# Performance work log

Hardware: AMD Instinct MI355X
Metric: run time of the kernel (lower is better)

## Reference

```python
import jax, jax.numpy as jnp
import numpy as np

IN_DIM = 128
LAYER_DIMS = [128, 128]
NUM_SAMPLES = [25, 10]
L0 = 3072
NEG_WEIGHT = 1.0


def setup_inputs() -> dict:
    key = jax.random.key(0)
    ks = jax.random.split(key, 12)
    feat = jax.random.normal(ks[0], (L0, IN_DIM), dtype=jnp.float32)
    nodes = jax.random.randint(ks[1], (L0,), 0, L0)
    nb0 = jnp.arange(L0)
    nb1 = jax.random.randint(ks[2], (L0 * 10,), 0, L0)
    nb2 = jax.random.randint(ks[3], (L0 * 10 * 25,), 0, L0)
    src_idx = jax.random.randint(ks[4], (1024,), 0, L0)
    pos_idx = jax.random.randint(ks[5], (1024,), 0, L0)
    neg_idx = jax.random.randint(ks[6], (512,), 0, L0)
    g = 0.05
    # mean aggregator weights: layer0 in=IN_DIM, layer1 in=2*128 (concat)
    w_self_0 = jax.random.normal(ks[7], (IN_DIM, 128), jnp.float32) * g
    w_neigh_0 = jax.random.normal(ks[8], (IN_DIM, 128), jnp.float32) * g
    w_self_1 = jax.random.normal(ks[9], (256, 128), jnp.float32) * g
    w_neigh_1 = jax.random.normal(ks[10], (256, 128), jnp.float32) * g
    return dict(nodes=nodes, feat=feat, src_idx=src_idx, pos_idx=pos_idx,
                neg_idx=neg_idx, nb0=nb0, nb1=nb1, nb2=nb2,
                w_self_0=w_self_0, w_neigh_0=w_neigh_0,
                w_self_1=w_self_1, w_neigh_1=w_neigh_1)


def _aggregate(hidden, params):
    # GraphSAGE layer stack: at layer l, combine each hop with the mean of its
    # sampled neighbors, concat self/neigh transforms, relu except last layer.
    num_layers = len(NUM_SAMPLES)
    for layer in range(num_layers):
        w_self, w_neigh = params[layer]
        is_last = layer == num_layers - 1
        next_hidden = []
        for hop in range(num_layers - layer):
            s = NUM_SAMPLES[num_layers - hop - 1]
            self_v = hidden[hop]  # [n, d]
            neigh = hidden[hop + 1].reshape(self_v.shape[0], s, self_v.shape[1])
            neigh_mean = jnp.mean(neigh, axis=1)
            h = jnp.concatenate([self_v @ w_self, neigh_mean @ w_neigh], axis=1)
            if not is_last:
                h = jax.nn.relu(h)
            next_hidden.append(h)
        hidden = next_hidden
    return hidden[0]


def _l2_normalize(x, eps=1e-12):
    return x * jax.lax.rsqrt(jnp.maximum(jnp.sum(x * x, axis=1, keepdims=True), eps))


def reference(nodes, feat, src_idx, pos_idx, neg_idx, nb0, nb1, nb2,
              w_self_0, w_neigh_0, w_self_1, w_neigh_1):
    hidden = [feat[nb0], feat[nb1], feat[nb2]]
    params = [(w_self_0, w_neigh_0), (w_self_1, w_neigh_1)]
    output = _aggregate(hidden, params)          # [L0, 256]
    output = _l2_normalize(output)
    src_emb = output[src_idx]                    # [B, 256]
    pos_emb = output[pos_idx]
    neg_emb = output[neg_idx]                    # [Nneg, 256]

    aff = jnp.sum(src_emb * pos_emb, axis=1)     # [B]
    neg_aff = src_emb @ neg_emb.T                # [B, Nneg]

    # MRR via double argsort (tf double top_k equivalent; ties -> positive last)
    aff_all = jnp.concatenate([neg_aff, aff[:, None]], axis=1)
    order = jnp.argsort(-aff_all, axis=1, stable=True)
    ranks = jnp.argsort(order, axis=1, stable=True)
    mrr = jnp.mean(1.0 / (ranks[:, -1].astype(jnp.float32) + 1.0))

    # sigmoid cross-entropy: labels 1 -> softplus(-x); labels 0 -> softplus(x)
    true_xent = jax.nn.softplus(-aff)
    neg_xent = jax.nn.softplus(neg_aff)
    loss = jnp.sum(true_xent) + NEG_WEIGHT * jnp.sum(neg_xent)
    loss = loss / jnp.asarray(src_emb.shape[0], jnp.float32)
    return src_emb, loss, mrr
```

## Files before the change

### kernel.cpp

```cpp
#include <hip/hip_runtime.h>
#include <math.h>

#define L0      3072
#define DIM     128
#define BATCH   1024
#define NNEG    512


__device__ __forceinline__ float bf2f(unsigned short u) {
  return __uint_as_float(((unsigned)u) << 16);
}
__device__ __forceinline__ void store_out(float v, float* p) { *p = v; }
__device__ __forceinline__ void store_out(float v, unsigned short* p) {
  unsigned x = __float_as_uint(v);
  *p = (unsigned short)((x + 0x7fff + ((x >> 16) & 1)) >> 16);
}

template<int K, int AW, int HOFF, bool NORM, typename OutT>
__global__ __launch_bounds__(256) void k_mm(
    const float* __restrict__ Ain,
    const float* __restrict__ W0, const float* __restrict__ W1,
    OutT* __restrict__ Out, const int ldo, const int outHalfOff,
    float* __restrict__ zbuf, const int zcount) {
  __shared__ float AT[6 * AW];
  __shared__ float rs[4][3];
  const int t = threadIdx.x;
  if (zbuf != nullptr && blockIdx.x == 0)
    for (int z = t; z < zcount; z += 256) zbuf[z] = 0.f;
  const int base = blockIdx.x * 6;
  {
    const float4* __restrict__ src = (const float4*)(Ain + base * AW);
    float4* __restrict__ dst = (float4*)AT;
    for (int idx = t; idx < 6 * AW / 4; idx += 256) dst[idx] = src[idx];
  }
  __syncthreads();

  const int half = t >> 7;
  const int rg = ((t >> 6) & 1) * 3;
  const int c = t & 63;
  const float* __restrict__ W = (half ? W1 : W0) + c;
  const float* __restrict__ A0 = AT + rg * AW + half * HOFF;

  float acc[3][2];
#pragma unroll
  for (int r = 0; r < 3; ++r) { acc[r][0] = 0.f; acc[r][1] = 0.f; }

#pragma unroll 4
  for (int d = 0; d < K; d += 4) {
    float4 a[3];
#pragma unroll
    for (int r = 0; r < 3; ++r) a[r] = *(const float4*)&A0[r * AW + d];
    float w0[4], w1[4];
#pragma unroll
    for (int i2 = 0; i2 < 4; ++i2) {
      w0[i2] = W[(d + i2) * 128];
      w1[i2] = W[(d + i2) * 128 + 64];
    }
#pragma unroll
    for (int i2 = 0; i2 < 4; ++i2)
#pragma unroll
      for (int r = 0; r < 3; ++r) {
        const float av = ((const float*)&a[r])[i2];
        acc[r][0] = fmaf(av, w0[i2], acc[r][0]);
        acc[r][1] = fmaf(av, w1[i2], acc[r][1]);
      }
  }

  float scale[3] = {1.f, 1.f, 1.f};
  if (NORM) {
    float p[3];
#pragma unroll
    for (int r = 0; r < 3; ++r) p[r] = acc[r][0] * acc[r][0] + acc[r][1] * acc[r][1];
#pragma unroll
    for (int off = 32; off > 0; off >>= 1)
#pragma unroll
      for (int r = 0; r < 3; ++r) p[r] += __shfl_xor(p[r], off, 64);
    const int wv = t >> 6;
    if ((t & 63) == 0) { rs[wv][0] = p[0]; rs[wv][1] = p[1]; rs[wv][2] = p[2]; }
    __syncthreads();
#pragma unroll
    for (int r = 0; r < 3; ++r) {
      const float s = (rg == 0) ? (rs[0][r] + rs[2][r]) : (rs[1][r] + rs[3][r]);
      scale[r] = rsqrtf(fmaxf(s, 1e-12f));
    }
  }
  OutT* __restrict__ O = Out + half * outHalfOff + c;
#pragma unroll
  for (int r = 0; r < 3; ++r) {
    store_out(acc[r][0] * scale[r], &O[(base + rg + r) * ldo]);
    store_out(acc[r][1] * scale[r], &O[(base + rg + r) * ldo + 64]);
  }
}

__global__ __launch_bounds__(640) void k_aggregate(
    const unsigned short* __restrict__ X0, const unsigned short* __restrict__ Y0,
    const int* __restrict__ nb0, const int* __restrict__ nb1,
    const int* __restrict__ nb2, float* __restrict__ H) {
  __shared__ int idxs[260];
  __shared__ float gB[10][128], gC[10][128], gD[10][128];
  const int i = blockIdx.x;
  const int t = threadIdx.x;
  if (t < 250) idxs[t] = nb2[i * 250 + t];
  else if (t < 260) idxs[t] = nb1[i * 10 + t - 250];
  __syncthreads();

  const int j = t >> 6;
  const int lam = t & 63;
  const int c8 = lam & 15;
  const int sub = lam >> 4;
  const int* __restrict__ pj = idxs + j * 25;

  float d8[8];
#pragma unroll
  for (int e = 0; e < 8; ++e) d8[e] = 0.f;
#pragma unroll
  for (int m = 0; m < 7; ++m) {
    const int k = sub + 4 * m;
    if (k < 25) {
      const int r = pj[k];
      const float4 raw = *(const float4*)(Y0 + r * 128 + c8 * 8);
      const unsigned short* u = (const unsigned short*)&raw;
#pragma unroll
      for (int e = 0; e < 8; ++e) d8[e] += bf2f(u[e]);
    }
  }
#pragma unroll
  for (int e = 0; e < 8; ++e) d8[e] += __shfl_xor(d8[e], 16, 64);
#pragma unroll
  for (int e = 0; e < 8; ++e) d8[e] += __shfl_xor(d8[e], 32, 64);

  const int r1 = idxs[250 + j];
  if (sub == 0) {
#pragma unroll
    for (int e = 0; e < 8; ++e) gD[j][c8 * 8 + e] = fmaxf(d8[e] * 0.04f, 0.f);
    const float4 raw = *(const float4*)(Y0 + r1 * 128 + c8 * 8);
    const unsigned short* u = (const unsigned short*)&raw;
#pragma unroll
    for (int e = 0; e < 8; ++e) gB[j][c8 * 8 + e] = bf2f(u[e]);
  } else if (sub == 1) {
    const float4 raw = *(const float4*)(X0 + r1 * 128 + c8 * 8);
    const unsigned short* u = (const unsigned short*)&raw;
#pragma unroll
    for (int e = 0; e < 8; ++e) gC[j][c8 * 8 + e] = fmaxf(bf2f(u[e]), 0.f);
  }
  __syncthreads();

  if (t < 512) {
    const int q = t >> 7, c = t & 127;
    float v;
    if (q == 0) {
      v = fmaxf(bf2f(X0[nb0[i] * 128 + c]), 0.f);
    } else {
      const float* g = (q == 1) ? &gB[0][0] : (q == 2) ? &gC[0][0] : &gD[0][0];
      float s = 0.f;
#pragma unroll
      for (int jj = 0; jj < 10; ++jj) s += g[jj * 128 + c];
      v = s * 0.1f;
      if (q == 1) v = fmaxf(v, 0.f);
    }
    H[i * 512 + t] = v;
  }
}

__device__ __forceinline__ float softplusf(float x) {
  return fmaxf(x, 0.f) + log1pf(expf(-fabsf(x)));
}

__global__ __launch_bounds__(64) void k_aff(
    const float* __restrict__ O, const int* __restrict__ src_idx,
    const int* __restrict__ pos_idx, float* __restrict__ out_src,
    float* __restrict__ aff, float* __restrict__ spPos) {
  __shared__ float4 sv[64], pv[64];
  const int b = blockIdx.x;
  const int q = threadIdx.x;
  const int s = src_idx[b];
  const int p = pos_idx[b];
  float4 vs = ((const float4*)O)[s * 64 + q];
  ((float4*)out_src)[b * 64 + q] = vs;
  sv[q] = vs;
  pv[q] = ((const float4*)O)[p * 64 + q];
  __syncthreads();
  if (q == 0) {
    const float* __restrict__ ss = (const float*)sv;
    const float* __restrict__ pp = (const float*)pv;
    float a = 0.f;
#pragma unroll 16
    for (int d = 0; d < 256; ++d) a = fmaf(ss[d], pp[d], a);
    aff[b] = a;
    atomicAdd(spPos, softplusf(-a));
  }
}

__global__ __launch_bounds__(256) void k_neg(
    const float* __restrict__ O, const int* __restrict__ src_idx,
    const int* __restrict__ neg_idx, const float* __restrict__ aff,
    int* __restrict__ rank, float* __restrict__ spNeg) {
  __shared__ float SL[32][129];
  __shared__ float NL[64][129];
  __shared__ float affL[32];
  __shared__ int cntL[32];
  const int t = threadIdx.x;
  const int rowBase = (blockIdx.x >> 3) * 32;
  const int colBase = (blockIdx.x & 7) * 64;
  if (t < 32) { affL[t] = aff[rowBase + t]; cntL[t] = 0; }
  const int ct = t & 31;
  const int rt = t >> 5;
  float acc[4][2];
#pragma unroll
  for (int k = 0; k < 4; ++k) { acc[k][0] = 0.f; acc[k][1] = 0.f; }
  for (int ch = 0; ch < 2; ++ch) {
    __syncthreads();
    for (int idx = t; idx < 32 * 128; idx += 256) {
      int r = idx >> 7, dd = idx & 127;
      SL[r][dd] = O[src_idx[rowBase + r] * 256 + ch * 128 + dd];
    }
    for (int idx = t; idx < 64 * 128; idx += 256) {
      int cpos = idx >> 7, dd = idx & 127;
      NL[cpos][dd] = O[neg_idx[colBase + cpos] * 256 + ch * 128 + dd];
    }
    __syncthreads();
    for (int dd = 0; dd < 128; ++dd) {
      float n0 = NL[ct][dd], n1 = NL[ct + 32][dd];
#pragma unroll
      for (int k = 0; k < 4; ++k) {
        float sv = SL[rt + 8 * k][dd];
        acc[k][0] = fmaf(sv, n0, acc[k][0]);
        acc[k][1] = fmaf(sv, n1, acc[k][1]);
      }
    }
  }
  float sp = 0.f;
#pragma unroll
  for (int k = 0; k < 4; ++k) {
    float a = affL[rt + 8 * k];
    int cnt = 0;
#pragma unroll
    for (int cc = 0; cc < 2; ++cc) {
      float v = acc[k][cc];
      sp += softplusf(v);
      cnt += (v >= a) ? 1 : 0;
    }
    if (cnt) atomicAdd(&cntL[rt + 8 * k], cnt);
  }
#pragma unroll
  for (int off = 32; off > 0; off >>= 1) sp += __shfl_down(sp, off, 64);
  if ((t & 63) == 0) atomicAdd(spNeg, sp);
  __syncthreads();
  if (t < 32) atomicAdd(&rank[rowBase + t], cntL[t]);
}

__global__ __launch_bounds__(256) void k_finalize(
    const int* __restrict__ rank, const float* __restrict__ spPos,
    const float* __restrict__ spNeg, float* __restrict__ out) {
  const int t = threadIdx.x;
  float s = 0.f;
  for (int i = t; i < BATCH; i += 256) s += 1.f / (float)(rank[i] + 1);
#pragma unroll
  for (int off = 32; off > 0; off >>= 1) s += __shfl_down(s, off, 64);
  __shared__ float wsum[4];
  if ((t & 63) == 0) wsum[t >> 6] = s;
  __syncthreads();
  if (t == 0) {
    float mrr = (wsum[0] + wsum[1] + wsum[2] + wsum[3]) * (1.f / 1024.f);
    float loss = (spPos[0] + spNeg[0]) * (1.f / 1024.f);
    out[BATCH * 256]     = loss;
    out[BATCH * 256 + 1] = mrr;
  }
}

extern "C" void kernel_launch(void* const* d_in, const int* in_sizes, int n_in,
                              void* d_out, int out_size, void* d_ws, size_t ws_size,
                              hipStream_t stream) {
  const float* feat   = (const float*)d_in[1];
  const int* src_idx  = (const int*)d_in[2];
  const int* pos_idx  = (const int*)d_in[3];
  const int* neg_idx  = (const int*)d_in[4];
  const int* nb0      = (const int*)d_in[5];
  const int* nb1      = (const int*)d_in[6];
  const int* nb2      = (const int*)d_in[7];
  const float* ws0    = (const float*)d_in[8];
  const float* wn0    = (const float*)d_in[9];
  const float* ws1    = (const float*)d_in[10];
  const float* wn1    = (const float*)d_in[11];

  float* wsf = (float*)d_ws;
  unsigned short* X0 = (unsigned short*)d_ws;
  unsigned short* Y0 = X0 + 393216;
  float* H     = wsf + 393216;
  float* R     = wsf + 1966080;
  float* aff   = wsf + 2752512;
  float* spPos = wsf + 2753536;
  float* spNeg = wsf + 2753537;
  int*   rank  = (int*)(wsf + 2753538);
  float* out   = (float*)d_out;

  k_mm<128, 128, 0, false, unsigned short><<<L0 / 6, 256, 0, stream>>>(
      feat, ws0, wn0, X0, 128, 393216, spPos, 1026);
  k_aggregate<<<L0, 640, 0, stream>>>(X0, Y0, nb0, nb1, nb2, H);
  k_mm<256, 512, 256, true, float><<<L0 / 6, 256, 0, stream>>>(
      H, ws1, wn1, R, 256, 128, nullptr, 0);
  k_aff<<<BATCH, 64, 0, stream>>>(R, src_idx, pos_idx, out, aff, spPos);
  k_neg<<<(BATCH / 32) * (NNEG / 64), 256, 0, stream>>>(R, src_idx, neg_idx, aff, rank, spNeg);
  k_finalize<<<1, 256, 0, stream>>>(rank, spPos, spNeg, out);
}
```

Before: 182.7 us.

## Fuse affinity kernel into k_neg, widen k_mm to 512 threads, shuffle indices

Removes the separate k_aff launch. Each k_neg block now recomputes the positive affinity for its 32 rows, and the first column block writes the src embeddings and accumulates the positive softplus. k_mm doubles its threads to 512, so each thread computes one output column instead of two, which raises parallelism and cuts registers per thread. k_aggregate replaces the shared-memory index staging and its barrier with per-wave register loads broadcast via __shfl. The cost is redundant affinity dot products across the 8 column blocks, done serially by 32 threads with strided global reads.

```diff
diff --git a/kernel.cpp b/kernel.cpp
--- a/kernel.cpp
+++ b/kernel.cpp
@@ -2,7 +2,6 @@
 #include <math.h>
 
 #define L0      3072
-#define DIM     128
 #define BATCH   1024
 #define NNEG    512
 
@@ -17,98 +16,88 @@
 }
 
 template<int K, int AW, int HOFF, bool NORM, typename OutT>
-__global__ __launch_bounds__(256) void k_mm(
+__global__ __launch_bounds__(512) void k_mm(
     const float* __restrict__ Ain,
     const float* __restrict__ W0, const float* __restrict__ W1,
     OutT* __restrict__ Out, const int ldo, const int outHalfOff,
     float* __restrict__ zbuf, const int zcount) {
   __shared__ float AT[6 * AW];
-  __shared__ float rs[4][3];
+  __shared__ float rs[8][3];
   const int t = threadIdx.x;
   if (zbuf != nullptr && blockIdx.x == 0)
-    for (int z = t; z < zcount; z += 256) zbuf[z] = 0.f;
+    for (int z = t; z < zcount; z += 512) zbuf[z] = 0.f;
   const int base = blockIdx.x * 6;
   {
     const float4* __restrict__ src = (const float4*)(Ain + base * AW);
     float4* __restrict__ dst = (float4*)AT;
-    for (int idx = t; idx < 6 * AW / 4; idx += 256) dst[idx] = src[idx];
-  }
-  __syncthreads();
-
-  const int half = t >> 7;
-  const int rg = ((t >> 6) & 1) * 3;
-  const int c = t & 63;
-  const float* __restrict__ W = (half ? W1 : W0) + c;
+    for (int idx = t; idx < 6 * AW / 4; idx += 512) dst[idx] = src[idx];
+  }
+  __syncthreads();
+
+  const int wave = t >> 6;
+  const int half = wave >> 2;
+  const int colg = (wave >> 1) & 1;
+  const int rowg = wave & 1;
+  const int rg = rowg * 3;
+  const int col = colg * 64 + (t & 63);
+  const float* __restrict__ W = (half ? W1 : W0) + col;
   const float* __restrict__ A0 = AT + rg * AW + half * HOFF;
 
-  float acc[3][2];
-#pragma unroll
-  for (int r = 0; r < 3; ++r) { acc[r][0] = 0.f; acc[r][1] = 0.f; }
-
+  float acc[3] = {0.f, 0.f, 0.f};
 #pragma unroll 4
   for (int d = 0; d < K; d += 4) {
     float4 a[3];
 #pragma unroll
     for (int r = 0; r < 3; ++r) a[r] = *(const float4*)&A0[r * AW + d];
-    float w0[4], w1[4];
-#pragma unroll
-    for (int i2 = 0; i2 < 4; ++i2) {
-      w0[i2] = W[(d + i2) * 128];
-      w1[i2] = W[(d + i2) * 128 + 64];
-    }
+    float w[4];
+#pragma unroll
+    for (int i2 = 0; i2 < 4; ++i2) w[i2] = W[(d + i2) * 128];
 #pragma unroll
     for (int i2 = 0; i2 < 4; ++i2)
 #pragma unroll
-      for (int r = 0; r < 3; ++r) {
-        const float av = ((const float*)&a[r])[i2];
-        acc[r][0] = fmaf(av, w0[i2], acc[r][0]);
-        acc[r][1] = fmaf(av, w1[i2], acc[r][1]);
-      }
+      for (int r = 0; r < 3; ++r)
+        acc[r] = fmaf(((const float*)&a[r])[i2], w[i2], acc[r]);
   }
 
   float scale[3] = {1.f, 1.f, 1.f};
   if (NORM) {
     float p[3];
 #pragma unroll
-    for (int r = 0; r < 3; ++r) p[r] = acc[r][0] * acc[r][0] + acc[r][1] * acc[r][1];
+    for (int r = 0; r < 3; ++r) p[r] = acc[r] * acc[r];
 #pragma unroll
     for (int off = 32; off > 0; off >>= 1)
 #pragma unroll
       for (int r = 0; r < 3; ++r) p[r] += __shfl_xor(p[r], off, 64);
-    const int wv = t >> 6;
-    if ((t & 63) == 0) { rs[wv][0] = p[0]; rs[wv][1] = p[1]; rs[wv][2] = p[2]; }
+    if ((t & 63) == 0) { rs[wave][0] = p[0]; rs[wave][1] = p[1]; rs[wave][2] = p[2]; }
     __syncthreads();
 #pragma unroll
     for (int r = 0; r < 3; ++r) {
-      const float s = (rg == 0) ? (rs[0][r] + rs[2][r]) : (rs[1][r] + rs[3][r]);
+      const float s = rs[rowg][r] + rs[rowg + 2][r] + rs[rowg + 4][r] + rs[rowg + 6][r];
       scale[r] = rsqrtf(fmaxf(s, 1e-12f));
     }
   }
-  OutT* __restrict__ O = Out + half * outHalfOff + c;
-#pragma unroll
-  for (int r = 0; r < 3; ++r) {
-    store_out(acc[r][0] * scale[r], &O[(base + rg + r) * ldo]);
-    store_out(acc[r][1] * scale[r], &O[(base + rg + r) * ldo + 64]);
-  }
+  OutT* __restrict__ O = Out + half * outHalfOff;
+#pragma unroll
+  for (int r = 0; r < 3; ++r)
+    store_out(acc[r] * scale[r], &O[(base + rg + r) * ldo + col]);
 }
 
 __global__ __launch_bounds__(640) void k_aggregate(
     const unsigned short* __restrict__ X0, const unsigned short* __restrict__ Y0,
     const int* __restrict__ nb0, const int* __restrict__ nb1,
     const int* __restrict__ nb2, float* __restrict__ H) {
-  __shared__ int idxs[260];
   __shared__ float gB[10][128], gC[10][128], gD[10][128];
   const int i = blockIdx.x;
   const int t = threadIdx.x;
-  if (t < 250) idxs[t] = nb2[i * 250 + t];
-  else if (t < 260) idxs[t] = nb1[i * 10 + t - 250];
-  __syncthreads();
-
+  const int n0 = nb0[i];
   const int j = t >> 6;
   const int lam = t & 63;
+  const int r = i * 10 + j;
+  int myidx = 0;
+  if (lam < 25) myidx = nb2[r * 25 + lam];
+  else if (lam == 25) myidx = nb1[r];
   const int c8 = lam & 15;
   const int sub = lam >> 4;
-  const int* __restrict__ pj = idxs + j * 25;
 
   float d8[8];
 #pragma unroll
@@ -116,9 +105,9 @@
 #pragma unroll
   for (int m = 0; m < 7; ++m) {
     const int k = sub + 4 * m;
+    const int ridx = __shfl(myidx, k, 64);
     if (k < 25) {
-      const int r = pj[k];
-      const float4 raw = *(const float4*)(Y0 + r * 128 + c8 * 8);
+      const float4 raw = *(const float4*)(Y0 + ridx * 128 + c8 * 8);
       const unsigned short* u = (const unsigned short*)&raw;
 #pragma unroll
       for (int e = 0; e < 8; ++e) d8[e] += bf2f(u[e]);
@@ -129,7 +118,7 @@
 #pragma unroll
   for (int e = 0; e < 8; ++e) d8[e] += __shfl_xor(d8[e], 32, 64);
 
-  const int r1 = idxs[250 + j];
+  const int r1 = __shfl(myidx, 25, 64);
   if (sub == 0) {
 #pragma unroll
     for (int e = 0; e < 8; ++e) gD[j][c8 * 8 + e] = fmaxf(d8[e] * 0.04f, 0.f);
@@ -149,7 +138,7 @@
     const int q = t >> 7, c = t & 127;
     float v;
     if (q == 0) {
-      v = fmaxf(bf2f(X0[nb0[i] * 128 + c]), 0.f);
+      v = fmaxf(bf2f(X0[n0 * 128 + c]), 0.f);
     } else {
       const float* g = (q == 1) ? &gB[0][0] : (q == 2) ? &gC[0][0] : &gD[0][0];
       float s = 0.f;
@@ -166,35 +155,11 @@
   return fmaxf(x, 0.f) + log1pf(expf(-fabsf(x)));
 }
 
-__global__ __launch_bounds__(64) void k_aff(
-    const float* __restrict__ O, const int* __restrict__ src_idx,
-    const int* __restrict__ pos_idx, float* __restrict__ out_src,
-    float* __restrict__ aff, float* __restrict__ spPos) {
-  __shared__ float4 sv[64], pv[64];
-  const int b = blockIdx.x;
-  const int q = threadIdx.x;
-  const int s = src_idx[b];
-  const int p = pos_idx[b];
-  float4 vs = ((const float4*)O)[s * 64 + q];
-  ((float4*)out_src)[b * 64 + q] = vs;
-  sv[q] = vs;
-  pv[q] = ((const float4*)O)[p * 64 + q];
-  __syncthreads();
-  if (q == 0) {
-    const float* __restrict__ ss = (const float*)sv;
-    const float* __restrict__ pp = (const float*)pv;
-    float a = 0.f;
-#pragma unroll 16
-    for (int d = 0; d < 256; ++d) a = fmaf(ss[d], pp[d], a);
-    aff[b] = a;
-    atomicAdd(spPos, softplusf(-a));
-  }
-}
-
 __global__ __launch_bounds__(256) void k_neg(
     const float* __restrict__ O, const int* __restrict__ src_idx,
-    const int* __restrict__ neg_idx, const float* __restrict__ aff,
-    int* __restrict__ rank, float* __restrict__ spNeg) {
+    const int* __restrict__ pos_idx, const int* __restrict__ neg_idx,
+    float* __restrict__ out_src, int* __restrict__ rank,
+    float* __restrict__ spPos, float* __restrict__ spNeg) {
   __shared__ float SL[32][129];
   __shared__ float NL[64][129];
   __shared__ float affL[32];
@@ -202,7 +167,25 @@
   const int t = threadIdx.x;
   const int rowBase = (blockIdx.x >> 3) * 32;
   const int colBase = (blockIdx.x & 7) * 64;
-  if (t < 32) { affL[t] = aff[rowBase + t]; cntL[t] = 0; }
+  const bool first = (colBase == 0);
+  if (t < 32) {
+    const int b = rowBase + t;
+    const float* __restrict__ ps = O + src_idx[b] * 256;
+    const float* __restrict__ pp = O + pos_idx[b] * 256;
+    float a = 0.f;
+#pragma unroll 16
+    for (int d = 0; d < 256; ++d) a = fmaf(ps[d], pp[d], a);
+    affL[t] = a;
+    cntL[t] = 0;
+    if (first) atomicAdd(spPos, softplusf(-a));
+  }
+  if (first) {
+    for (int idx = t; idx < 32 * 64; idx += 256) {
+      const int rr = idx >> 6, qq = idx & 63;
+      ((float4*)out_src)[(rowBase + rr) * 64 + qq] =
+          ((const float4*)O)[src_idx[rowBase + rr] * 64 + qq];
+    }
+  }
   const int ct = t & 31;
   const int rt = t >> 5;
   float acc[4][2];
@@ -288,18 +271,17 @@
   unsigned short* Y0 = X0 + 393216;
   float* H     = wsf + 393216;
   float* R     = wsf + 1966080;
-  float* aff   = wsf + 2752512;
-  float* spPos = wsf + 2753536;
-  float* spNeg = wsf + 2753537;
-  int*   rank  = (int*)(wsf + 2753538);
+  float* spPos = wsf + 2752512;
+  float* spNeg = wsf + 2752513;
+  int*   rank  = (int*)(wsf + 2752514);
   float* out   = (float*)d_out;
 
-  k_mm<128, 128, 0, false, unsigned short><<<L0 / 6, 256, 0, stream>>>(
+  k_mm<128, 128, 0, false, unsigned short><<<L0 / 6, 512, 0, stream>>>(
       feat, ws0, wn0, X0, 128, 393216, spPos, 1026);
   k_aggregate<<<L0, 640, 0, stream>>>(X0, Y0, nb0, nb1, nb2, H);
-  k_mm<256, 512, 256, true, float><<<L0 / 6, 256, 0, stream>>>(
+  k_mm<256, 512, 256, true, float><<<L0 / 6, 512, 0, stream>>>(
       H, ws1, wn1, R, 256, 128, nullptr, 0);
-  k_aff<<<BATCH, 64, 0, stream>>>(R, src_idx, pos_idx, out, aff, spPos);
-  k_neg<<<(BATCH / 32) * (NNEG / 64), 256, 0, stream>>>(R, src_idx, neg_idx, aff, rank, spNeg);
+  k_neg<<<(BATCH / 32) * (NNEG / 64), 256, 0, stream>>>(
+      R, src_idx, pos_idx, neg_idx, out, rank, spPos, spNeg);
   k_finalize<<<1, 256, 0, stream>>>(rank, spPos, spNeg, out);
 }
```

Measured after the change: 165.4 us. -9.5%, faster.
